# Kernel tuning notes

Hardware: AMD Instinct MI355X
Metric: run time of the kernel (lower is better)

Reference implementation:

```python
import jax, jax.numpy as jnp
import numpy as np

PROP_TIME = 8  # matches init_kwargs prop_time


def _patches(x, dil):
    # x: [B,1,H,W] -> [B,9,H,W]; 'same' padding with the given dilation,
    # matching torch.nn.functional.unfold(kernel_size=3, dilation=dil, padding=dil).
    return jax.lax.conv_general_dilated_patches(
        x,
        filter_shape=(3, 3),
        window_strides=(1, 1),
        padding=[(dil, dil), (dil, dil)],
        rhs_dilation=(dil, dil),
    )


def setup_inputs() -> dict:
    key = jax.random.key(0)
    k1, k2, k3, k4 = jax.random.split(key, 4)
    B, H, W = 4, 352, 1216
    guided1 = jax.random.normal(k1, (B, 9, H, W), dtype=jnp.float32)
    guided2 = jax.random.normal(k2, (B, 9, H, W), dtype=jnp.float32)
    fuse = jax.random.uniform(k3, (B, 2, H, W), dtype=jnp.float32)
    x = jax.random.normal(k4, (B, 1, H, W), dtype=jnp.float32)
    return {"guided1": guided1, "guided2": guided2, "fuse": fuse, "x": x}


def reference(guided1, guided2, fuse, x):
    # softmax over the 9 kernel taps -> spatially varying normalized kernels
    kern1 = jax.nn.softmax(guided1, axis=1)  # [B,9,H,W]
    kern2 = jax.nn.softmax(guided2, axis=1)  # [B,9,H,W]
    f1 = fuse[:, 0:1]  # [B,1,H,W]
    f2 = fuse[:, 1:2]
    for _ in range(PROP_TIME):
        p1 = _patches(x, 1)  # [B,9,H,W]
        p2 = _patches(x, 2)
        o1 = jnp.sum(p1 * kern1, axis=1, keepdims=True)  # [B,1,H,W]
        o2 = jnp.sum(p2 * kern2, axis=1, keepdims=True)
        x = o1 * f1 + o2 * f2
    return x
```

## Files before the change

### kernel.cpp

```cpp
#include <hip/hip_runtime.h>

#define HH 352
#define WW 1216
#define NB 4
#define HWSZ (HH * WW)
#define WQ 304
#define BHQ (HH * WQ)
#define NQ (NB * BHQ)

typedef _Float16 half4 __attribute__((ext_vector_type(4)));
typedef _Float16 half8 __attribute__((ext_vector_type(8)));


__global__ __launch_bounds__(256, 4) void softmax_prop1_kernel(
    const float* __restrict__ g1, const float* __restrict__ g2,
    const float* __restrict__ fuse, const float* __restrict__ x0,
    _Float16* __restrict__ kk, _Float16* __restrict__ x1) {
    int q = blockIdx.x * 256 + threadIdx.x;
    if (q >= NQ) return;
    int b   = q / BHQ;
    int rem = q - b * BHQ;
    int h   = rem / WQ;
    int wq  = rem - h * WQ;
    int w0  = wq * 4;
    long gbase = (long)b * 9 * HWSZ + (long)rem * 4;
    long fbase = (long)b * 2 * HWSZ + (long)rem * 4;

    float4 t[18];
#pragma unroll
    for (int k = 0; k < 9; k++) t[k]     = *(const float4*)(g1 + gbase + (long)k * HWSZ);
#pragma unroll
    for (int k = 0; k < 9; k++) t[9 + k] = *(const float4*)(g2 + gbase + (long)k * HWSZ);
    float4 f1 = *(const float4*)(fuse + fbase);
    float4 f2 = *(const float4*)(fuse + fbase + HWSZ);

    float s1[4] = {0.f, 0.f, 0.f, 0.f}, s2[4] = {0.f, 0.f, 0.f, 0.f};
#pragma unroll
    for (int k = 0; k < 9; k++) {
        t[k].x = __expf(t[k].x); s1[0] += t[k].x;
        t[k].y = __expf(t[k].y); s1[1] += t[k].y;
        t[k].z = __expf(t[k].z); s1[2] += t[k].z;
        t[k].w = __expf(t[k].w); s1[3] += t[k].w;
    }
#pragma unroll
    for (int k = 9; k < 18; k++) {
        t[k].x = __expf(t[k].x); s2[0] += t[k].x;
        t[k].y = __expf(t[k].y); s2[1] += t[k].y;
        t[k].z = __expf(t[k].z); s2[2] += t[k].z;
        t[k].w = __expf(t[k].w); s2[3] += t[k].w;
    }
    float r1[4], r2[4];
    r1[0] = f1.x / s1[0]; r1[1] = f1.y / s1[1]; r1[2] = f1.z / s1[2]; r1[3] = f1.w / s1[3];
    r2[0] = f2.x / s2[0]; r2[1] = f2.y / s2[1]; r2[2] = f2.z / s2[2]; r2[3] = f2.w / s2[3];

    long obase = gbase * 2;
    half8 kv[9];
#pragma unroll
    for (int k = 0; k < 9; k++) {
        half8 o;
        o[0] = (_Float16)(t[k].x * r1[0]); o[1] = (_Float16)(t[9 + k].x * r2[0]);
        o[2] = (_Float16)(t[k].y * r1[1]); o[3] = (_Float16)(t[9 + k].y * r2[1]);
        o[4] = (_Float16)(t[k].z * r1[2]); o[5] = (_Float16)(t[9 + k].z * r2[2]);
        o[6] = (_Float16)(t[k].w * r1[3]); o[7] = (_Float16)(t[9 + k].w * r2[3]);
        kv[k] = o;
        *(half8*)(kk + obase + (long)k * HWSZ * 2) = o;
    }

    const float* xb = x0 + (long)b * HWSZ;
    float rb[5][8];
#pragma unroll
    for (int r = 0; r < 5; r++) {
        int hh = h - 2 + r;
        bool rv = (hh >= 0) && (hh < HH);
        const float* rp = xb + (long)hh * WW;
        float4 mid = rv ? *(const float4*)(rp + w0) : make_float4(0.f, 0.f, 0.f, 0.f);
        float2 lft = (rv && w0 > 0) ? *(const float2*)(rp + w0 - 2) : make_float2(0.f, 0.f);
        float2 rgt = (rv && (w0 + 5) < WW) ? *(const float2*)(rp + w0 + 4) : make_float2(0.f, 0.f);
        rb[r][0] = lft.x; rb[r][1] = lft.y;
        rb[r][2] = mid.x; rb[r][3] = mid.y; rb[r][4] = mid.z; rb[r][5] = mid.w;
        rb[r][6] = rgt.x; rb[r][7] = rgt.y;
    }
    float o[4] = {0.f, 0.f, 0.f, 0.f};
#pragma unroll
    for (int ky = 0; ky < 3; ky++)
#pragma unroll
        for (int kx = 0; kx < 3; kx++) {
            int k = ky * 3 + kx;
#pragma unroll
            for (int j = 0; j < 4; j++) {
                o[j] = fmaf((float)kv[k][2 * j],     rb[ky + 1][j + 1 + kx], o[j]);
                o[j] = fmaf((float)kv[k][2 * j + 1], rb[2 * ky][j + 2 * kx], o[j]);
            }
        }
    half4 xo;
    xo[0] = (_Float16)o[0]; xo[1] = (_Float16)o[1];
    xo[2] = (_Float16)o[2]; xo[3] = (_Float16)o[3];
    *(half4*)(x1 + (long)b * HWSZ + (long)rem * 4) = xo;
}

#define TW 64
#define TH 4
#define LW (TW + 2)
#define LROWS (TH + 4)
#define TILES_W 5
#define TILES_H (HH / TH)

template <int OUT16>
__global__ __launch_bounds__(256, 4) void prop_kernel(
    const _Float16* __restrict__ kk,
    const _Float16* __restrict__ xin, void* __restrict__ xout_) {
    __shared__ float xs[LROWS][LW * 4];

    int tid = threadIdx.x;
    int bidx = blockIdx.x;
    int tX = bidx % TILES_W;
    int r1 = bidx / TILES_W;
    int tY = r1 % TILES_H;
    int b  = r1 / TILES_H;
    int q0 = tX * TW;
    int h0 = tY * TH;

    const _Float16* xb = xin + (long)b * HWSZ;

#pragma unroll
    for (int i = tid; i < LROWS * LW; i += 256) {
        int row = i / LW;
        int qc  = i - row * LW;
        int h   = h0 - 2 + row;
        int qg  = q0 - 1 + qc;
        float4 v = make_float4(0.f, 0.f, 0.f, 0.f);
        if (h >= 0 && h < HH && qg >= 0 && qg < WQ) {
            half4 hv = *(const half4*)(xb + (long)h * WW + qg * 4);
            v = make_float4((float)hv[0], (float)hv[1], (float)hv[2], (float)hv[3]);
        }
        *(float4*)&xs[row][qc * 4] = v;
    }
    __syncthreads();

    int tx = tid & (TW - 1);
    int ty = tid >> 6;
    int qa = q0 + tx;
    if (qa >= WQ) return;

    int h = h0 + ty;
    long p0 = (long)h * WW + qa * 4;
    long kbase = ((long)b * 9 * HWSZ + p0) * 2;

    half8 kv[9];
#pragma unroll
    for (int k = 0; k < 9; k++)
        kv[k] = *(const half8*)(kk + kbase + (long)k * HWSZ * 2);

    float rb[5][8];
#pragma unroll
    for (int r = 0; r < 5; r++) {
        const float* p = &xs[ty + r][4 * tx + 2];
        float2 a = *(const float2*)(p);
        float4 m = *(const float4*)(p + 2);
        float2 z = *(const float2*)(p + 6);
        rb[r][0] = a.x; rb[r][1] = a.y;
        rb[r][2] = m.x; rb[r][3] = m.y; rb[r][4] = m.z; rb[r][5] = m.w;
        rb[r][6] = z.x; rb[r][7] = z.y;
    }

    float o[4] = {0.f, 0.f, 0.f, 0.f};
#pragma unroll
    for (int ky = 0; ky < 3; ky++)
#pragma unroll
        for (int kx = 0; kx < 3; kx++) {
            int k = ky * 3 + kx;
#pragma unroll
            for (int j = 0; j < 4; j++) {
                o[j] = fmaf((float)kv[k][2 * j],     rb[ky + 1][j + 1 + kx], o[j]);
                o[j] = fmaf((float)kv[k][2 * j + 1], rb[2 * ky][j + 2 * kx], o[j]);
            }
        }

    if (OUT16) {
        half4 xo;
        xo[0] = (_Float16)o[0]; xo[1] = (_Float16)o[1];
        xo[2] = (_Float16)o[2]; xo[3] = (_Float16)o[3];
        *(half4*)((_Float16*)xout_ + (long)b * HWSZ + p0) = xo;
    } else {
        *(float4*)((float*)xout_ + (long)b * HWSZ + p0) =
            make_float4(o[0], o[1], o[2], o[3]);
    }
}

extern "C" void kernel_launch(void* const* d_in, const int* in_sizes, int n_in,
                              void* d_out, int out_size, void* d_ws, size_t ws_size,
                              hipStream_t stream) {
    const float* g1   = (const float*)d_in[0];
    const float* g2   = (const float*)d_in[1];
    const float* fuse = (const float*)d_in[2];
    const float* x    = (const float*)d_in[3];
    float* out = (float*)d_out;

    _Float16* kk   = (_Float16*)d_ws;
    _Float16* bufA = kk + (size_t)NB * 9 * HWSZ * 2;
    _Float16* bufB = bufA + (size_t)NB * HWSZ;

    int sm_blocks = (NQ + 255) / 256;
    softmax_prop1_kernel<<<sm_blocks, 256, 0, stream>>>(g1, g2, fuse, x, kk, bufA);

    int pr_blocks = NB * TILES_H * TILES_W;
    prop_kernel<1><<<pr_blocks, 256, 0, stream>>>(kk, bufA, bufB);
    prop_kernel<1><<<pr_blocks, 256, 0, stream>>>(kk, bufB, bufA);
    prop_kernel<1><<<pr_blocks, 256, 0, stream>>>(kk, bufA, bufB);
    prop_kernel<1><<<pr_blocks, 256, 0, stream>>>(kk, bufB, bufA);
    prop_kernel<1><<<pr_blocks, 256, 0, stream>>>(kk, bufA, bufB);
    prop_kernel<1><<<pr_blocks, 256, 0, stream>>>(kk, bufB, bufA);
    prop_kernel<0><<<pr_blocks, 256, 0, stream>>>(kk, bufA, out);
}
```

Measured before the change: 246.6 us.

## Fuse softmax and all propagation steps into one persistent cooperative kernel

Replaces the eight separate launches with one cooperative persistent kernel of 1024 blocks. Each block owns up to two tiles and keeps their softmax-normalized kernel weights in registers across all iterations, so the fp16 kernel buffer is never written or re-read. Iterations are separated by a hand-written two-level atomic grid barrier. This removes repeated global traffic for the weights and per-launch overhead, at the cost of register pressure from holding two tiles of weights, barrier latency, and a dependency on all blocks being co-resident.

```diff
diff --git a/kernel.cpp b/kernel.cpp
--- a/kernel.cpp
+++ b/kernel.cpp
@@ -8,9 +8,218 @@
 #define BHQ (HH * WQ)
 #define NQ (NB * BHQ)
 
+#define TW 64
+#define TH 4
+#define LW (TW + 2)
+#define LROWS (TH + 4)
+#define TILES_W 5
+#define TILES_H (HH / TH)
+#define NTILES (NB * TILES_H * TILES_W)
+#define GBLK 1024
+#define BANDS 8
+#define PER_BAND (GBLK / BANDS)
+#define TPB (NTILES / BANDS)
+
 typedef _Float16 half4 __attribute__((ext_vector_type(4)));
 typedef _Float16 half8 __attribute__((ext_vector_type(8)));
 
+__device__ __forceinline__ void gsync(unsigned* sy, int band, unsigned target) {
+    __syncthreads();
+    if (threadIdx.x == 0) {
+        unsigned* cnt  = sy + band * 64;
+        unsigned* root = sy + 512;
+        unsigned* gen  = sy + 640;
+        unsigned old = __hip_atomic_fetch_add(cnt, 1u, __ATOMIC_ACQ_REL,
+                                              __HIP_MEMORY_SCOPE_AGENT);
+        if (old == PER_BAND - 1u) {
+            __hip_atomic_store(cnt, 0u, __ATOMIC_RELAXED, __HIP_MEMORY_SCOPE_AGENT);
+            unsigned r = __hip_atomic_fetch_add(root, 1u, __ATOMIC_ACQ_REL,
+                                                __HIP_MEMORY_SCOPE_AGENT);
+            if (r == BANDS - 1u) {
+                __hip_atomic_store(root, 0u, __ATOMIC_RELAXED, __HIP_MEMORY_SCOPE_AGENT);
+                __hip_atomic_store(gen, target, __ATOMIC_RELEASE, __HIP_MEMORY_SCOPE_AGENT);
+            } else {
+                while (__hip_atomic_load(gen, __ATOMIC_ACQUIRE,
+                                         __HIP_MEMORY_SCOPE_AGENT) < target)
+                    __builtin_amdgcn_s_sleep(4);
+            }
+        } else {
+            while (__hip_atomic_load(gen, __ATOMIC_ACQUIRE,
+                                     __HIP_MEMORY_SCOPE_AGENT) < target)
+                __builtin_amdgcn_s_sleep(4);
+        }
+    }
+    __syncthreads();
+}
+
+#define SOFTMAX_TILE(tv, actT, bT, p0T) do {                                   \
+    if (actT) {                                                                \
+        const long _gb = (long)(bT) * 9 * HWSZ + (p0T);                        \
+        float _s1[4] = {0.f,0.f,0.f,0.f}, _s2[4] = {0.f,0.f,0.f,0.f};          \
+        _Pragma("unroll")                                                      \
+        for (int _k = 0; _k < 9; _k++) {                                       \
+            float4 _a = *(const float4*)(g1 + _gb + (long)_k * HWSZ);          \
+            float4 _c = *(const float4*)(g2 + _gb + (long)_k * HWSZ);          \
+            _a.x = __expf(_a.x); _a.y = __expf(_a.y);                          \
+            _a.z = __expf(_a.z); _a.w = __expf(_a.w);                          \
+            _c.x = __expf(_c.x); _c.y = __expf(_c.y);                          \
+            _c.z = __expf(_c.z); _c.w = __expf(_c.w);                          \
+            _s1[0] += _a.x; _s1[1] += _a.y; _s1[2] += _a.z; _s1[3] += _a.w;    \
+            _s2[0] += _c.x; _s2[1] += _c.y; _s2[2] += _c.z; _s2[3] += _c.w;    \
+            half8 _o;                                                          \
+            _o[0] = (_Float16)_a.x; _o[1] = (_Float16)_c.x;                    \
+            _o[2] = (_Float16)_a.y; _o[3] = (_Float16)_c.y;                    \
+            _o[4] = (_Float16)_a.z; _o[5] = (_Float16)_c.z;                    \
+            _o[6] = (_Float16)_a.w; _o[7] = (_Float16)_c.w;                    \
+            tv[_k] = _o;                                                       \
+        }                                                                      \
+        const long _fb = (long)(bT) * 2 * HWSZ + (p0T);                        \
+        float4 _f1 = *(const float4*)(fuse + _fb);                             \
+        float4 _f2 = *(const float4*)(fuse + _fb + HWSZ);                      \
+        float _r1[4], _r2[4];                                                  \
+        _r1[0] = _f1.x / _s1[0]; _r1[1] = _f1.y / _s1[1];                      \
+        _r1[2] = _f1.z / _s1[2]; _r1[3] = _f1.w / _s1[3];                      \
+        _r2[0] = _f2.x / _s2[0]; _r2[1] = _f2.y / _s2[1];                      \
+        _r2[2] = _f2.z / _s2[2]; _r2[3] = _f2.w / _s2[3];                      \
+        _Pragma("unroll")                                                      \
+        for (int _k = 0; _k < 9; _k++) {                                       \
+            half8 _o = tv[_k];                                                 \
+            _Pragma("unroll")                                                  \
+            for (int _j = 0; _j < 4; _j++) {                                   \
+                _o[2*_j]   = (_Float16)((float)_o[2*_j]   * _r1[_j]);          \
+                _o[2*_j+1] = (_Float16)((float)_o[2*_j+1] * _r2[_j]);          \
+            }                                                                  \
+            tv[_k] = _o;                                                       \
+        }                                                                      \
+    }                                                                          \
+} while (0)
+
+#define STAGE_TILE(xs, bT, h0T, q0T) do {                                      \
+    const float*    _xb32 = x0  + (long)(bT) * HWSZ;                           \
+    const _Float16* _xb16 = cur + (long)(bT) * HWSZ;                           \
+    for (int _i = tid; _i < LROWS * LW; _i += 256) {                           \
+        int _row = _i / LW;                                                    \
+        int _qc  = _i - _row * LW;                                             \
+        int _hh  = (h0T) - 2 + _row;                                           \
+        int _qg  = (q0T) - 1 + _qc;                                            \
+        float4 _v = make_float4(0.f, 0.f, 0.f, 0.f);                           \
+        if (_hh >= 0 && _hh < HH && _qg >= 0 && _qg < WQ) {                    \
+            if (s == 1) {                                                      \
+                _v = *(const float4*)(_xb32 + (long)_hh * WW + _qg * 4);       \
+            } else {                                                           \
+                half4 _hv = *(const half4*)(_xb16 + (long)_hh * WW + _qg * 4); \
+                _v = make_float4((float)_hv[0], (float)_hv[1],                 \
+                                 (float)_hv[2], (float)_hv[3]);                \
+            }                                                                  \
+        }                                                                      \
+        *(float4*)&xs[_row][_qc * 4] = _v;                                     \
+    }                                                                          \
+} while (0)
+
+#define COMPUTE_TILE(xs, tv, actT, obaseT) do {                                \
+    if (actT) {                                                                \
+        float _oo[4] = {0.f, 0.f, 0.f, 0.f};                                   \
+        _Pragma("unroll")                                                      \
+        for (int _r = 0; _r < 5; _r++) {                                       \
+            const float* _p = &xs[ty + _r][4 * tx + 2];                        \
+            float2 _aa = *(const float2*)(_p);                                 \
+            float4 _mm = *(const float4*)(_p + 2);                             \
+            float2 _zz = *(const float2*)(_p + 6);                             \
+            float _rw[8] = {_aa.x, _aa.y, _mm.x, _mm.y,                        \
+                            _mm.z, _mm.w, _zz.x, _zz.y};                       \
+            if (_r >= 1 && _r <= 3) {                                          \
+                const int _ky = _r - 1;                                        \
+                _Pragma("unroll")                                              \
+                for (int _kx = 0; _kx < 3; _kx++) {                            \
+                    const int _k = _ky * 3 + _kx;                              \
+                    _Pragma("unroll")                                          \
+                    for (int _j = 0; _j < 4; _j++)                             \
+                        _oo[_j] = fmaf((float)tv[_k][2*_j],                    \
+                                       _rw[_j + 1 + _kx], _oo[_j]);            \
+                }                                                              \
+            }                                                                  \
+            if ((_r & 1) == 0) {                                               \
+                const int _ky = _r >> 1;                                       \
+                _Pragma("unroll")                                              \
+                for (int _kx = 0; _kx < 3; _kx++) {                            \
+                    const int _k = _ky * 3 + _kx;                              \
+                    _Pragma("unroll")                                          \
+                    for (int _j = 0; _j < 4; _j++)                             \
+                        _oo[_j] = fmaf((float)tv[_k][2*_j+1],                  \
+                                       _rw[_j + 2*_kx], _oo[_j]);              \
+                }                                                              \
+            }                                                                  \
+        }                                                                      \
+        if (s < 8) {                                                           \
+            half4 _xo;                                                         \
+            _xo[0] = (_Float16)_oo[0]; _xo[1] = (_Float16)_oo[1];              \
+            _xo[2] = (_Float16)_oo[2]; _xo[3] = (_Float16)_oo[3];              \
+            *(half4*)(nxt + (obaseT)) = _xo;                                   \
+        } else {                                                               \
+            *(float4*)(out + (obaseT)) =                                       \
+                make_float4(_oo[0], _oo[1], _oo[2], _oo[3]);                   \
+        }                                                                      \
+    }                                                                          \
+} while (0)
+
+__global__ __launch_bounds__(256, 4) void fused_all(
+    const float* __restrict__ g1, const float* __restrict__ g2,
+    const float* __restrict__ fuse, const float* __restrict__ x0,
+    float* __restrict__ out, _Float16* __restrict__ bufA,
+    _Float16* __restrict__ bufB, unsigned* __restrict__ sy)
+{
+    __shared__ float xsA[LROWS][LW * 4];
+    __shared__ float xsB[LROWS][LW * 4];
+
+    const int tid  = threadIdx.x;
+    const int bid  = blockIdx.x;
+    const int band = bid & 7;
+    const int idx  = bid >> 3;
+
+    const int tx = tid & (TW - 1);
+    const int ty = tid >> 6;
+
+    const int tileA = band * TPB + idx;
+    int tXA = tileA % TILES_W; int rrA = tileA / TILES_W;
+    int tYA = rrA % TILES_H;   int bA  = rrA / TILES_H;
+    int q0A = tXA * TW, h0A = tYA * TH;
+    int qaA = q0A + tx; const bool actA = (qaA < WQ);
+    int p0A = (h0A + ty) * WW + qaA * 4;
+    int obaseA = bA * HWSZ + p0A;
+
+    const bool hasB = (PER_BAND + idx) < TPB;
+    const int tileB = band * TPB + (hasB ? (PER_BAND + idx) : idx);
+    int tXB = tileB % TILES_W; int rrB = tileB / TILES_W;
+    int tYB = rrB % TILES_H;   int bB  = rrB / TILES_H;
+    int q0B = tXB * TW, h0B = tYB * TH;
+    int qaB = q0B + tx; const bool actB = hasB && (qaB < WQ);
+    int p0B = (h0B + ty) * WW + qaB * 4;
+    int obaseB = bB * HWSZ + p0B;
+
+    half8 tvA[9], tvB[9];
+    SOFTMAX_TILE(tvA, actA, bA, p0A);
+    if (hasB) SOFTMAX_TILE(tvB, actB, bB, p0B);
+
+    const _Float16* cur = bufA;
+    _Float16* nxt = bufA;
+
+#pragma unroll 1
+    for (int s = 1; s <= 8; ++s) {
+        STAGE_TILE(xsA, bA, h0A, q0A);
+        if (hasB) STAGE_TILE(xsB, bB, h0B, q0B);
+        __syncthreads();
+
+        COMPUTE_TILE(xsA, tvA, actA, obaseA);
+        if (hasB) COMPUTE_TILE(xsB, tvB, actB, obaseB);
+
+        if (s < 8) gsync(sy, band, (unsigned)s);
+        else break;
+
+        cur = nxt;
+        nxt = (cur == bufA) ? bufB : bufA;
+        __syncthreads();
+    }
+}
 
 __global__ __launch_bounds__(256, 4) void softmax_prop1_kernel(
     const float* __restrict__ g1, const float* __restrict__ g2,
@@ -98,13 +307,6 @@
     *(half4*)(x1 + (long)b * HWSZ + (long)rem * 4) = xo;
 }
 
-#define TW 64
-#define TH 4
-#define LW (TW + 2)
-#define LROWS (TH + 4)
-#define TILES_W 5
-#define TILES_H (HH / TH)
-
 template <int OUT16>
 __global__ __launch_bounds__(256, 4) void prop_kernel(
     const _Float16* __restrict__ kk,
@@ -199,6 +401,17 @@
     _Float16* kk   = (_Float16*)d_ws;
     _Float16* bufA = kk + (size_t)NB * 9 * HWSZ * 2;
     _Float16* bufB = bufA + (size_t)NB * HWSZ;
+    unsigned* sy   = (unsigned*)d_ws;
+
+    hipError_t err = hipMemsetAsync(sy, 0, 4096, stream);
+    if (err == hipSuccess) {
+        void* args[] = {(void*)&g1, (void*)&g2, (void*)&fuse, (void*)&x,
+                        (void*)&out, (void*)&bufA, (void*)&bufB, (void*)&sy};
+        err = hipLaunchCooperativeKernel(
+            reinterpret_cast<void*>(fused_all), dim3(GBLK), dim3(256), args, 0, stream);
+        if (err == hipSuccess) return;
+    }
+    (void)hipGetLastError();
 
     int sm_blocks = (NQ + 255) / 256;
     softmax_prop1_kernel<<<sm_blocks, 256, 0, stream>>>(g1, g2, fuse, x, kk, bufA);
```

Result: slower. 885.1 us (+258.9%).

## Fuse two propagation steps per kernel using shared-memory halo recompute

Applied to the files above, without the earlier changes.

Adds prop2_kernel, which loads a wider x halo tile into shared memory, computes an intermediate step over an extended region into a second shared buffer, then computes the next step from that. Six single-step launches become three double-step launches plus one final single step, which halves the launch count and the intermediate x traffic. The cost is redundant halo computation and extra reads of the kernel weights for halo pixels, since kk is loaded for the extended region, along with a larger shared-memory footprint.

```diff
diff --git a/kernel.cpp b/kernel.cpp
--- a/kernel.cpp
+++ b/kernel.cpp
@@ -10,7 +10,6 @@
 
 typedef _Float16 half4 __attribute__((ext_vector_type(4)));
 typedef _Float16 half8 __attribute__((ext_vector_type(8)));
-
 
 __global__ __launch_bounds__(256, 4) void softmax_prop1_kernel(
     const float* __restrict__ g1, const float* __restrict__ g2,
@@ -187,6 +186,127 @@
     }
 }
 
+#define DTW 64
+#define DTH 8
+#define DXW (DTW + 4)
+#define DSR (DTH + 8)
+#define DIW (DTW + 2)
+#define DIR (DTH + 4)
+#define DTILES_W 5
+#define DTILES_H (HH / DTH)
+
+#define CONV9(XS, RB, CB, KV, OO) do {                                         \
+    _Pragma("unroll")                                                          \
+    for (int _r = 0; _r < 5; _r++) {                                           \
+        const float* _p = &XS[(RB) + _r][(CB)];                                \
+        float2 _aa = *(const float2*)(_p);                                     \
+        float4 _mm = *(const float4*)(_p + 2);                                 \
+        float2 _zz = *(const float2*)(_p + 6);                                 \
+        float _rw[8] = {_aa.x, _aa.y, _mm.x, _mm.y,                            \
+                        _mm.z, _mm.w, _zz.x, _zz.y};                           \
+        if (_r >= 1 && _r <= 3) {                                              \
+            const int _ky = _r - 1;                                            \
+            _Pragma("unroll")                                                  \
+            for (int _kx = 0; _kx < 3; _kx++) {                                \
+                const int _k = _ky * 3 + _kx;                                  \
+                _Pragma("unroll")                                              \
+                for (int _j = 0; _j < 4; _j++)                                 \
+                    OO[_j] = fmaf((float)KV[_k][2 * _j],                       \
+                                  _rw[_j + 1 + _kx], OO[_j]);                  \
+            }                                                                  \
+        }                                                                      \
+        if ((_r & 1) == 0) {                                                   \
+            const int _ky = _r >> 1;                                           \
+            _Pragma("unroll")                                                  \
+            for (int _kx = 0; _kx < 3; _kx++) {                                \
+                const int _k = _ky * 3 + _kx;                                  \
+                _Pragma("unroll")                                              \
+                for (int _j = 0; _j < 4; _j++)                                 \
+                    OO[_j] = fmaf((float)KV[_k][2 * _j + 1],                   \
+                                  _rw[_j + 2 * _kx], OO[_j]);                  \
+            }                                                                  \
+        }                                                                      \
+    }                                                                          \
+} while (0)
+
+template <int OUT16>
+__global__ __launch_bounds__(256, 4) void prop2_kernel(
+    const _Float16* __restrict__ kk,
+    const _Float16* __restrict__ xin, void* __restrict__ xout_) {
+    __shared__ float xs0[DSR][DXW * 4];
+    __shared__ float xs1[DIR][DIW * 4];
+
+    const int tid  = threadIdx.x;
+    const int bidx = blockIdx.x;
+    const int tX = bidx % DTILES_W;
+    const int r1 = bidx / DTILES_W;
+    const int tY = r1 % DTILES_H;
+    const int b  = r1 / DTILES_H;
+    const int q0 = tX * DTW;
+    const int h0 = tY * DTH;
+
+    const _Float16* xb = xin + (long)b * HWSZ;
+    const _Float16* kb = kk + (long)b * 9 * HWSZ * 2;
+
+    for (int i = tid; i < DSR * DXW; i += 256) {
+        int row = i / DXW;
+        int qc  = i - row * DXW;
+        int h   = h0 - 4 + row;
+        int qg  = q0 - 2 + qc;
+        float4 v = make_float4(0.f, 0.f, 0.f, 0.f);
+        if (h >= 0 && h < HH && qg >= 0 && qg < WQ) {
+            half4 hv = *(const half4*)(xb + (long)h * WW + qg * 4);
+            v = make_float4((float)hv[0], (float)hv[1], (float)hv[2], (float)hv[3]);
+        }
+        *(float4*)&xs0[row][qc * 4] = v;
+    }
+    __syncthreads();
+
+    for (int t = tid; t < DIR * DIW; t += 256) {
+        int tr = t / DIW;
+        int qc = t - tr * DIW;
+        int h  = h0 - 2 + tr;
+        int qg = q0 - 1 + qc;
+        float oo[4] = {0.f, 0.f, 0.f, 0.f};
+        if (h >= 0 && h < HH && qg >= 0 && qg < WQ) {
+            long p = (long)h * WW + qg * 4;
+            half8 kv[9];
+#pragma unroll
+            for (int k = 0; k < 9; k++)
+                kv[k] = *(const half8*)(kb + p * 2 + (long)k * HWSZ * 2);
+            CONV9(xs0, tr, 4 * qc + 2, kv, oo);
+        }
+        *(float4*)&xs1[tr][qc * 4] = make_float4(oo[0], oo[1], oo[2], oo[3]);
+    }
+    __syncthreads();
+
+    for (int t = tid; t < DTH * DTW; t += 256) {
+        int tr = t >> 6;
+        int qc = t & (DTW - 1);
+        int qg = q0 + qc;
+        if (qg >= WQ) continue;
+        int h  = h0 + tr;
+        long p = (long)h * WW + qg * 4;
+        half8 kv[9];
+#pragma unroll
+        for (int k = 0; k < 9; k++)
+            kv[k] = *(const half8*)(kb + p * 2 + (long)k * HWSZ * 2);
+        float oo[4] = {0.f, 0.f, 0.f, 0.f};
+        CONV9(xs1, tr, 4 * qc + 2, kv, oo);
+
+        long ob = (long)b * HWSZ + p;
+        if (OUT16) {
+            half4 xo;
+            xo[0] = (_Float16)oo[0]; xo[1] = (_Float16)oo[1];
+            xo[2] = (_Float16)oo[2]; xo[3] = (_Float16)oo[3];
+            *(half4*)((_Float16*)xout_ + ob) = xo;
+        } else {
+            *(float4*)((float*)xout_ + ob) =
+                make_float4(oo[0], oo[1], oo[2], oo[3]);
+        }
+    }
+}
+
 extern "C" void kernel_launch(void* const* d_in, const int* in_sizes, int n_in,
                               void* d_out, int out_size, void* d_ws, size_t ws_size,
                               hipStream_t stream) {
@@ -203,12 +323,11 @@
     int sm_blocks = (NQ + 255) / 256;
     softmax_prop1_kernel<<<sm_blocks, 256, 0, stream>>>(g1, g2, fuse, x, kk, bufA);
 
+    int p2_blocks = NB * DTILES_H * DTILES_W;
+    prop2_kernel<1><<<p2_blocks, 256, 0, stream>>>(kk, bufA, bufB);
+    prop2_kernel<1><<<p2_blocks, 256, 0, stream>>>(kk, bufB, bufA);
+    prop2_kernel<1><<<p2_blocks, 256, 0, stream>>>(kk, bufA, bufB);
+
     int pr_blocks = NB * TILES_H * TILES_W;
-    prop_kernel<1><<<pr_blocks, 256, 0, stream>>>(kk, bufA, bufB);
-    prop_kernel<1><<<pr_blocks, 256, 0, stream>>>(kk, bufB, bufA);
-    prop_kernel<1><<<pr_blocks, 256, 0, stream>>>(kk, bufA, bufB);
-    prop_kernel<1><<<pr_blocks, 256, 0, stream>>>(kk, bufB, bufA);
-    prop_kernel<1><<<pr_blocks, 256, 0, stream>>>(kk, bufA, bufB);
-    prop_kernel<1><<<pr_blocks, 256, 0, stream>>>(kk, bufB, bufA);
-    prop_kernel<0><<<pr_blocks, 256, 0, stream>>>(kk, bufA, out);
+    prop_kernel<0><<<pr_blocks, 256, 0, stream>>>(kk, bufB, out);
 }
```

Result: slower. 263.0 us (+6.7%).
